# Kernel tuning notes

Hardware: AMD Instinct MI355X
Metric: run time of the kernel (lower is better)

Reference implementation:

```python
import jax, jax.numpy as jnp
from jax import lax
import numpy as np

D_X, D_Y, HID = 64, 1, 128
D_NODES = D_X + 2          # d_x + 2
D_IN = D_X + 1 + D_Y       # fc_in input dim
K_LANGEVIN, ETA = 20, 0.01
BATCH = 8192


def setup_inputs() -> dict:
    key = jax.random.key(0)
    ks = jax.random.split(key, 12)
    s = 0.05
    return {
        "x": jax.random.normal(ks[0], (BATCH, D_X), jnp.float32),
        "t": jnp.ones((BATCH, 1), jnp.float32),
        "B_param": s * jax.random.normal(ks[1], (D_NODES, D_NODES), jnp.float32),
        "W_in": s * jax.random.normal(ks[2], (D_IN, HID), jnp.float32),
        "b_in": jnp.zeros((HID,), jnp.float32),
        "WT1": s * jax.random.normal(ks[3], (HID, HID), jnp.float32),
        "bT1": jnp.zeros((HID,), jnp.float32),
        "WT2": s * jax.random.normal(ks[4], (HID, 1), jnp.float32),
        "bT2": jnp.zeros((1,), jnp.float32),
        "WY1": s * jax.random.normal(ks[5], (HID, HID), jnp.float32),
        "bY1": jnp.zeros((HID,), jnp.float32),
        "WY2": s * jax.random.normal(ks[6], (HID, 1), jnp.float32),
        "bY2": jnp.zeros((1,), jnp.float32),
    }


def _mask():
    m = jnp.ones((D_NODES, D_NODES), jnp.float32)
    m = m.at[-1, :D_X].set(0.0)          # last node has no incoming edges from x-nodes
    m = m * (1.0 - jnp.eye(D_NODES, dtype=jnp.float32))  # zero diagonal
    return m


def _energy(z, x, B_param, mask, W_in, b_in, WT1, bT1, WT2, bT2, WY1, bY1, WY2, bY2):
    # z = [t, y] : [B, 1 + d_y]
    A = jax.nn.sigmoid(B_param) * mask                       # [N, N]
    h0 = jnp.concatenate([x, z], axis=-1) @ W_in + b_in      # [B, H]
    h = jnp.broadcast_to(h0[:, None, :], (h0.shape[0], D_NODES, HID))  # repeat over nodes
    # MaskedGraphConv: h + (A @ h) / d_nodes, then ReLU (x2)
    h = jax.nn.relu(h + jnp.einsum('ij,bjd->bid', A, h) / D_NODES)
    h = jax.nn.relu(h + jnp.einsum('ij,bjd->bid', A, h) / D_NODES)
    eT = jax.nn.relu(h[:, -2] @ WT1 + bT1) @ WT2 + bT2       # [B, 1]
    eY = jax.nn.relu(h[:, -1] @ WY1 + bY1) @ WY2 + bY2       # [B, 1]
    return (eT + eY)[:, 0]                                   # [B]


def reference(x, t, B_param, W_in, b_in, WT1, bT1, WT2, bT2, WY1, bY1, WY2, bY2):
    mask = _mask()
    grad_E = jax.grad(lambda z: _energy(z, x, B_param, mask, W_in, b_in,
                                        WT1, bT1, WT2, bT2, WY1, bY1, WY2, bY2).sum())
    z0 = jnp.concatenate([t, jnp.zeros((x.shape[0], D_Y), x.dtype)], axis=-1)
    sqrt_eta = jnp.sqrt(jnp.float32(ETA))

    def step(z, k):
        g = grad_E(z)
        noise = jax.random.normal(k, z.shape, z.dtype)
        return z - 0.5 * ETA * g + sqrt_eta * noise, None

    keys = jax.random.split(jax.random.key(42), K_LANGEVIN)
    z_final, _ = lax.scan(step, z0, keys)
    return z_final[:, 1:]   # predicted y, [B, d_y]
```

## Files before the change

### kernel.cpp

```cpp
#include <hip/hip_runtime.h>
#include <stdint.h>

#define NBATCH 8192
#define HID    128
#define DXC    64
#define NN     66
#define NSTEP  20
#define MROWS  16
#define RSTR   136
#define DSTR   280

typedef __attribute__((ext_vector_type(8))) short short8;
typedef __attribute__((ext_vector_type(4))) float f32x4;

static __device__ __forceinline__ ushort f2bf(float f) {
  union { float f; uint32_t u; } v; v.f = f;
  uint32_t u = v.u;
  u += 0x7fffu + ((u >> 16) & 1u);
  return (ushort)(u >> 16);
}

__device__ __forceinline__ void tf2x32(uint32_t k1, uint32_t k2,
                                       uint32_t x0, uint32_t x1,
                                       uint32_t &o0, uint32_t &o1) {
  uint32_t k3 = k1 ^ k2 ^ 0x1BD11BDAu;
  x0 += k1; x1 += k2;
#define RND(r) do { x0 += x1; x1 = (x1 << (r)) | (x1 >> (32 - (r))); x1 ^= x0; } while (0)
  RND(13); RND(15); RND(26); RND(6);
  x0 += k2; x1 += k3 + 1u;
  RND(17); RND(29); RND(16); RND(24);
  x0 += k3; x1 += k1 + 2u;
  RND(13); RND(15); RND(26); RND(6);
  x0 += k1; x1 += k2 + 3u;
  RND(17); RND(29); RND(16); RND(24);
  x0 += k2; x1 += k3 + 4u;
  RND(13); RND(15); RND(26); RND(6);
  x0 += k3; x1 += k1 + 5u;
#undef RND
  o0 = x0; o1 = x1;
}

__device__ __forceinline__ float erfinv_f(float x) {
  float w = -log1pf(-x * x);
  float p1, p2;
  {
    float ww = w - 2.5f;
    float p = 2.81022636e-08f;
    p = fmaf(p, ww, 3.43273939e-07f);
    p = fmaf(p, ww, -3.5233877e-06f);
    p = fmaf(p, ww, -4.39150654e-06f);
    p = fmaf(p, ww, 0.00021858087f);
    p = fmaf(p, ww, -0.00125372503f);
    p = fmaf(p, ww, -0.00417768164f);
    p = fmaf(p, ww, 0.246640727f);
    p = fmaf(p, ww, 1.50140941f);
    p1 = p;
  }
  {
    float ww = sqrtf(w) - 3.0f;
    float p = -0.000200214257f;
    p = fmaf(p, ww, 0.000100950558f);
    p = fmaf(p, ww, 0.00134934322f);
    p = fmaf(p, ww, -0.00367342844f);
    p = fmaf(p, ww, 0.00573950773f);
    p = fmaf(p, ww, -0.0076224613f);
    p = fmaf(p, ww, 0.00943887047f);
    p = fmaf(p, ww, 1.00167406f);
    p = fmaf(p, ww, 2.83297682f);
    p2 = p;
  }
  float p = (w < 5.0f) ? p1 : p2;
  return p * x;
}

__device__ __forceinline__ float bits_to_normal(uint32_t bits) {
  float f = __uint_as_float((bits >> 9) | 0x3F800000u) - 1.0f;
  const float LO = -0.99999994f;
  float u = fmaxf(LO, fmaf(f, 2.0f, LO));
  return 1.41421356237f * erfinv_f(u);
}

__global__ __launch_bounds__(256) void prep_frags(const float* __restrict__ Bp,
                                                  const float* __restrict__ WT1,
                                                  const float* __restrict__ WY1,
                                                  ushort* __restrict__ frag) {
  __shared__ float cb[NN];
  __shared__ float dsc[2];
  int tid = threadIdx.x;
  if (tid < NN) {
    float rs = 0.f;
    for (int j = 0; j < NN; ++j) {
      if (j == tid) continue;
      if (tid == NN - 1 && j < DXC) continue;
      float v = Bp[tid * NN + j];
      rs += 1.f / (1.f + expf(-v));
    }
    cb[tid] = 1.f + rs / 66.f;
  }
  __syncthreads();
  if (tid < 2) {
    int i = 64 + tid;
    float s = 0.f;
    for (int j = 0; j < NN; ++j) {
      if (j == i) continue;
      if (i == NN - 1 && j < DXC) continue;
      float v = Bp[i * NN + j];
      s += (1.f / (1.f + expf(-v))) * cb[j];
    }
    dsc[tid] = cb[i] + s / 66.f;
  }
  __syncthreads();
  float d64 = dsc[0], d65 = dsc[1];

  int g = blockIdx.x * 256 + tid;
  int lane = g & 63, kt = (g >> 6) & 3, c = (g >> 8) & 7, mi = g >> 11;
  int r16 = lane & 15, q = lane >> 4;
  int bcol = c * 16 + r16;
  const float* W = (mi == 0 || mi == 2) ? WT1 : WY1;
  float d = (mi == 0 || mi == 2) ? d64 : d65;
  bool fwd = (mi < 2);
  ushort v[8];
#pragma unroll
  for (int j = 0; j < 8; ++j) {
    int a = kt * 32 + q * 8 + j;
    float val = fwd ? W[a * HID + bcol] : W[bcol * HID + a];
    v[j] = f2bf(d * val);
  }
  uint4 st;
  st.x = (uint32_t)v[0] | ((uint32_t)v[1] << 16);
  st.y = (uint32_t)v[2] | ((uint32_t)v[3] << 16);
  st.z = (uint32_t)v[4] | ((uint32_t)v[5] << 16);
  st.w = (uint32_t)v[6] | ((uint32_t)v[7] << 16);
  ((uint4*)frag)[g] = st;
}

__global__ __launch_bounds__(256, 2) void ebm_langevin(
    const float* __restrict__ x, const float* __restrict__ t_in,
    const float* __restrict__ W_in, const float* __restrict__ b_in,
    const float* __restrict__ bT1, const float* __restrict__ WT2,
    const float* __restrict__ bY1, const float* __restrict__ WY2,
    const ushort* __restrict__ fragw,
    float* __restrict__ out) {

  __shared__ __align__(16) ushort rT[MROWS * RSTR];
  __shared__ __align__(16) ushort duL[MROWS * DSTR];
  __shared__ float xs[MROWS * DXC];
  __shared__ float zt[MROWS], zy[MROWS];
  __shared__ float gpart[4][MROWS][2];
  __shared__ uint32_t skeys[NSTEP][2];

  const int tid  = threadIdx.x;
  const int lane = tid & 63;
  const int wv   = tid >> 6;
  const int r16  = lane & 15;
  const int q    = lane >> 4;
  const int brow0 = blockIdx.x * MROWS;

  const short8* fragp = reinterpret_cast<const short8*>(fragw);

  const int c0 = 2 * wv, c1 = 2 * wv + 1;
  const int n0 = c0 * 16 + r16, n1 = c1 * 16 + r16;
  const float bT1a = bT1[n0], bT1b = bT1[n1];
  const float bY1a = bY1[n0], bY1b = bY1[n1];
  const ushort wT2a = f2bf(WT2[n0]), wT2b = f2bf(WT2[n1]);
  const ushort wY2a = f2bf(WY2[n0]), wY2b = f2bf(WY2[n1]);
  const float wtA = W_in[64 * HID + n0], wtB = W_in[64 * HID + n1];
  const float wyA = W_in[65 * HID + n0], wyB = W_in[65 * HID + n1];

  const float2 wtk2 = ((const float2*)(W_in + 64 * HID))[lane];
  const float2 wyk2 = ((const float2*)(W_in + 65 * HID))[lane];

  ((float4*)xs)[tid] = ((const float4*)(x + (size_t)brow0 * DXC))[tid];
  if (tid < MROWS) { zt[tid] = t_in[brow0 + tid]; zy[tid] = 0.f; }
  if (tid < NSTEP) {
    uint32_t o0, o1;
    tf2x32(0u, 42u, 0u, (uint32_t)tid, o0, o1);
    skeys[tid][0] = o0; skeys[tid][1] = o1;
  }
  __syncthreads();

  float h0x_[4][2];
  {
    float2 b2 = ((const float2*)b_in)[lane];
#pragma unroll
    for (int m = 0; m < 4; ++m) { h0x_[m][0] = b2.x; h0x_[m][1] = b2.y; }
    for (int cc = 0; cc < DXC; ++cc) {
      float2 w2 = ((const float2*)(W_in + cc * HID))[lane];
#pragma unroll
      for (int m = 0; m < 4; ++m) {
        float xv = xs[(wv * 4 + m) * DXC + cc];
        h0x_[m][0] = fmaf(xv, w2.x, h0x_[m][0]);
        h0x_[m][1] = fmaf(xv, w2.y, h0x_[m][1]);
      }
    }
  }
  __syncthreads();

  for (int s = 0; s < NSTEP; ++s) {
#pragma unroll
    for (int m = 0; m < 4; ++m) {
      int mg = wv * 4 + m;
      float ztv = zt[mg], zyv = zy[mg];
      float h0 = fmaf(zyv, wyk2.x, fmaf(ztv, wtk2.x, h0x_[m][0]));
      float h1 = fmaf(zyv, wyk2.y, fmaf(ztv, wtk2.y, h0x_[m][1]));
      ushort lo = f2bf(fmaxf(h0, 0.f));
      ushort hi = f2bf(fmaxf(h1, 0.f));
      ((uint32_t*)rT)[mg * (RSTR / 2) + lane] = (uint32_t)lo | ((uint32_t)hi << 16);
    }
    __syncthreads();

    {
      short8 ar[4];
#pragma unroll
      for (int kt = 0; kt < 4; ++kt)
        ar[kt] = *reinterpret_cast<const short8*>(&rT[r16 * RSTR + kt * 32 + q * 8]);

      f32x4 aT0 = {0.f, 0.f, 0.f, 0.f}, aT1 = aT0, aY0 = aT0, aY1 = aT0;
#pragma unroll
      for (int kt = 0; kt < 4; ++kt) {
        aT0 = __builtin_amdgcn_mfma_f32_16x16x32_bf16(ar[kt], fragp[((0 * 8 + c0) * 4 + kt) * 64 + lane], aT0, 0, 0, 0);
        aT1 = __builtin_amdgcn_mfma_f32_16x16x32_bf16(ar[kt], fragp[((0 * 8 + c1) * 4 + kt) * 64 + lane], aT1, 0, 0, 0);
        aY0 = __builtin_amdgcn_mfma_f32_16x16x32_bf16(ar[kt], fragp[((1 * 8 + c0) * 4 + kt) * 64 + lane], aY0, 0, 0, 0);
        aY1 = __builtin_amdgcn_mfma_f32_16x16x32_bf16(ar[kt], fragp[((1 * 8 + c1) * 4 + kt) * 64 + lane], aY1, 0, 0, 0);
      }
#pragma unroll
      for (int reg = 0; reg < 4; ++reg) {
        int row = q * 4 + reg;
        duL[row * DSTR + n0]       = (aT0[reg] + bT1a > 0.f) ? wT2a : (ushort)0;
        duL[row * DSTR + n1]       = (aT1[reg] + bT1b > 0.f) ? wT2b : (ushort)0;
        duL[row * DSTR + 128 + n0] = (aY0[reg] + bY1a > 0.f) ? wY2a : (ushort)0;
        duL[row * DSTR + 128 + n1] = (aY1[reg] + bY1b > 0.f) ? wY2b : (ushort)0;
      }
    }
    __syncthreads();

    {
      short8 dt[4], dy[4];
#pragma unroll
      for (int kt = 0; kt < 4; ++kt) {
        dt[kt] = *reinterpret_cast<const short8*>(&duL[r16 * DSTR + kt * 32 + q * 8]);
        dy[kt] = *reinterpret_cast<const short8*>(&duL[r16 * DSTR + 128 + kt * 32 + q * 8]);
      }
      f32x4 g0 = {0.f, 0.f, 0.f, 0.f}, g1 = g0;
#pragma unroll
      for (int kt = 0; kt < 4; ++kt) {
        g0 = __builtin_amdgcn_mfma_f32_16x16x32_bf16(dt[kt], fragp[((2 * 8 + c0) * 4 + kt) * 64 + lane], g0, 0, 0, 0);
        g1 = __builtin_amdgcn_mfma_f32_16x16x32_bf16(dt[kt], fragp[((2 * 8 + c1) * 4 + kt) * 64 + lane], g1, 0, 0, 0);
      }
#pragma unroll
      for (int kt = 0; kt < 4; ++kt) {
        g0 = __builtin_amdgcn_mfma_f32_16x16x32_bf16(dy[kt], fragp[((3 * 8 + c0) * 4 + kt) * 64 + lane], g0, 0, 0, 0);
        g1 = __builtin_amdgcn_mfma_f32_16x16x32_bf16(dy[kt], fragp[((3 * 8 + c1) * 4 + kt) * 64 + lane], g1, 0, 0, 0);
      }
      float pt[4], py[4];
#pragma unroll
      for (int reg = 0; reg < 4; ++reg) {
        int row = q * 4 + reg;
        short rv0 = (short)rT[row * RSTR + n0];
        short rv1 = (short)rT[row * RSTR + n1];
        float v0 = (rv0 > 0) ? g0[reg] : 0.f;
        float v1 = (rv1 > 0) ? g1[reg] : 0.f;
        pt[reg] = fmaf(v0, wtA, v1 * wtB);
        py[reg] = fmaf(v0, wyA, v1 * wyB);
      }
#pragma unroll
      for (int reg = 0; reg < 4; ++reg) {
#pragma unroll
        for (int off = 1; off < 16; off <<= 1) {
          pt[reg] += __shfl_xor(pt[reg], off);
          py[reg] += __shfl_xor(py[reg], off);
        }
      }
      if (r16 == 0) {
#pragma unroll
        for (int reg = 0; reg < 4; ++reg) {
          gpart[wv][q * 4 + reg][0] = pt[reg];
          gpart[wv][q * 4 + reg][1] = py[reg];
        }
      }
    }
    __syncthreads();

    if (tid < MROWS) {
      float gt = gpart[0][tid][0] + gpart[1][tid][0] + gpart[2][tid][0] + gpart[3][tid][0];
      float gy = gpart[0][tid][1] + gpart[1][tid][1] + gpart[2][tid][1] + gpart[3][tid][1];
      uint32_t idx = (uint32_t)(2 * (brow0 + tid));
      uint32_t o0, o1;
      tf2x32(skeys[s][0], skeys[s][1], 0u, idx, o0, o1);
      float nt = bits_to_normal(o0 ^ o1);
      tf2x32(skeys[s][0], skeys[s][1], 0u, idx + 1u, o0, o1);
      float ny = bits_to_normal(o0 ^ o1);
      zt[tid] = (zt[tid] - 0.005f * gt) + 0.1f * nt;
      zy[tid] = (zy[tid] - 0.005f * gy) + 0.1f * ny;
    }
    __syncthreads();
  }

  if (tid < MROWS) out[brow0 + tid] = zy[tid];
}

extern "C" void kernel_launch(void* const* d_in, const int* in_sizes, int n_in,
                              void* d_out, int out_size, void* d_ws, size_t ws_size,
                              hipStream_t stream) {
  const float* x    = (const float*)d_in[0];
  const float* t_in = (const float*)d_in[1];
  const float* Bp   = (const float*)d_in[2];
  const float* W_in = (const float*)d_in[3];
  const float* b_in = (const float*)d_in[4];
  const float* WT1  = (const float*)d_in[5];
  const float* bT1  = (const float*)d_in[6];
  const float* WT2  = (const float*)d_in[7];
  const float* WY1  = (const float*)d_in[9];
  const float* bY1  = (const float*)d_in[10];
  const float* WY2  = (const float*)d_in[11];
  float* out = (float*)d_out;
  ushort* frag = (ushort*)d_ws;

  prep_frags<<<64, 256, 0, stream>>>(Bp, WT1, WY1, frag);
  ebm_langevin<<<NBATCH / MROWS, 256, 0, stream>>>(
      x, t_in, W_in, b_in, bT1, WT2, bY1, WY2, frag, out);
}
```

Measured before the change: 168.8 us.

## Fuse weight-fragment prep into Langevin kernel and hold B-fragments in registers

Removes the separate prep_frags launch. Every block now computes the graph-conv scale factors from B_param and builds its bf16 MFMA B-fragments for WT1/WY1 (forward and transposed) directly into registers, instead of reloading them from a global workspace on every Langevin step. This drops one kernel launch and the per-step global fragment loads. In exchange it adds redundant per-block sigmoid and weight-conversion work, 32 short8 registers per thread that may hurt occupancy or spill, and uncoalesced strided reads of WT1/WY1.

```diff
diff --git a/kernel.cpp b/kernel.cpp
--- a/kernel.cpp
+++ b/kernel.cpp
@@ -80,13 +80,39 @@
   return 1.41421356237f * erfinv_f(u);
 }
 
-__global__ __launch_bounds__(256) void prep_frags(const float* __restrict__ Bp,
-                                                  const float* __restrict__ WT1,
-                                                  const float* __restrict__ WY1,
-                                                  ushort* __restrict__ frag) {
+__global__ __launch_bounds__(256, 2) void ebm_fused(
+    const float* __restrict__ x, const float* __restrict__ t_in,
+    const float* __restrict__ Bp,
+    const float* __restrict__ W_in, const float* __restrict__ b_in,
+    const float* __restrict__ WT1, const float* __restrict__ bT1,
+    const float* __restrict__ WT2,
+    const float* __restrict__ WY1, const float* __restrict__ bY1,
+    const float* __restrict__ WY2,
+    float* __restrict__ out) {
+
+  __shared__ __align__(16) ushort rT[MROWS * RSTR];
+  __shared__ __align__(16) ushort duL[MROWS * DSTR];
+  __shared__ float xs[MROWS * DXC];
+  __shared__ float zt[MROWS], zy[MROWS];
+  __shared__ float gpart[4][MROWS][2];
+  __shared__ uint32_t skeys[NSTEP][2];
   __shared__ float cb[NN];
   __shared__ float dsc[2];
-  int tid = threadIdx.x;
+
+  const int tid  = threadIdx.x;
+  const int lane = tid & 63;
+  const int wv   = tid >> 6;
+  const int r16  = lane & 15;
+  const int q    = lane >> 4;
+  const int brow0 = blockIdx.x * MROWS;
+
+  ((float4*)xs)[tid] = ((const float4*)(x + (size_t)brow0 * DXC))[tid];
+  if (tid < MROWS) { zt[tid] = t_in[brow0 + tid]; zy[tid] = 0.f; }
+  if (tid < NSTEP) {
+    uint32_t o0, o1;
+    tf2x32(0u, 42u, 0u, (uint32_t)tid, o0, o1);
+    skeys[tid][0] = o0; skeys[tid][1] = o1;
+  }
   if (tid < NN) {
     float rs = 0.f;
     for (int j = 0; j < NN; ++j) {
@@ -110,74 +136,46 @@
     dsc[tid] = cb[i] + s / 66.f;
   }
   __syncthreads();
-  float d64 = dsc[0], d65 = dsc[1];
-
-  int g = blockIdx.x * 256 + tid;
-  int lane = g & 63, kt = (g >> 6) & 3, c = (g >> 8) & 7, mi = g >> 11;
-  int r16 = lane & 15, q = lane >> 4;
-  int bcol = c * 16 + r16;
-  const float* W = (mi == 0 || mi == 2) ? WT1 : WY1;
-  float d = (mi == 0 || mi == 2) ? d64 : d65;
-  bool fwd = (mi < 2);
-  ushort v[8];
-#pragma unroll
-  for (int j = 0; j < 8; ++j) {
-    int a = kt * 32 + q * 8 + j;
-    float val = fwd ? W[a * HID + bcol] : W[bcol * HID + a];
-    v[j] = f2bf(d * val);
-  }
-  uint4 st;
-  st.x = (uint32_t)v[0] | ((uint32_t)v[1] << 16);
-  st.y = (uint32_t)v[2] | ((uint32_t)v[3] << 16);
-  st.z = (uint32_t)v[4] | ((uint32_t)v[5] << 16);
-  st.w = (uint32_t)v[6] | ((uint32_t)v[7] << 16);
-  ((uint4*)frag)[g] = st;
-}
-
-__global__ __launch_bounds__(256, 2) void ebm_langevin(
-    const float* __restrict__ x, const float* __restrict__ t_in,
-    const float* __restrict__ W_in, const float* __restrict__ b_in,
-    const float* __restrict__ bT1, const float* __restrict__ WT2,
-    const float* __restrict__ bY1, const float* __restrict__ WY2,
-    const ushort* __restrict__ fragw,
-    float* __restrict__ out) {
-
-  __shared__ __align__(16) ushort rT[MROWS * RSTR];
-  __shared__ __align__(16) ushort duL[MROWS * DSTR];
-  __shared__ float xs[MROWS * DXC];
-  __shared__ float zt[MROWS], zy[MROWS];
-  __shared__ float gpart[4][MROWS][2];
-  __shared__ uint32_t skeys[NSTEP][2];
-
-  const int tid  = threadIdx.x;
-  const int lane = tid & 63;
-  const int wv   = tid >> 6;
-  const int r16  = lane & 15;
-  const int q    = lane >> 4;
-  const int brow0 = blockIdx.x * MROWS;
-
-  const short8* fragp = reinterpret_cast<const short8*>(fragw);
-
-  const int c0 = 2 * wv, c1 = 2 * wv + 1;
-  const int n0 = c0 * 16 + r16, n1 = c1 * 16 + r16;
+  const float d64 = dsc[0], d65 = dsc[1];
+
+  const int n0 = 32 * wv + r16, n1 = n0 + 16;
   const float bT1a = bT1[n0], bT1b = bT1[n1];
   const float bY1a = bY1[n0], bY1b = bY1[n1];
   const ushort wT2a = f2bf(WT2[n0]), wT2b = f2bf(WT2[n1]);
   const ushort wY2a = f2bf(WY2[n0]), wY2b = f2bf(WY2[n1]);
   const float wtA = W_in[64 * HID + n0], wtB = W_in[64 * HID + n1];
   const float wyA = W_in[65 * HID + n0], wyB = W_in[65 * HID + n1];
-
   const float2 wtk2 = ((const float2*)(W_in + 64 * HID))[lane];
   const float2 wyk2 = ((const float2*)(W_in + 65 * HID))[lane];
 
-  ((float4*)xs)[tid] = ((const float4*)(x + (size_t)brow0 * DXC))[tid];
-  if (tid < MROWS) { zt[tid] = t_in[brow0 + tid]; zy[tid] = 0.f; }
-  if (tid < NSTEP) {
-    uint32_t o0, o1;
-    tf2x32(0u, 42u, 0u, (uint32_t)tid, o0, o1);
-    skeys[tid][0] = o0; skeys[tid][1] = o1;
-  }
-  __syncthreads();
+  short8 fT0[4], fT1[4], fY0[4], fY1[4];
+  short8 hT0[4], hT1[4], hY0[4], hY1[4];
+#pragma unroll
+  for (int kt = 0; kt < 4; ++kt) {
+    const int kb = kt * 32 + q * 8;
+    short8 a0, a1, b0, b1;
+#pragma unroll
+    for (int j = 0; j < 8; ++j) {
+      a0[j] = (short)f2bf(d64 * WT1[(kb + j) * HID + n0]);
+      a1[j] = (short)f2bf(d64 * WT1[(kb + j) * HID + n1]);
+      b0[j] = (short)f2bf(d65 * WY1[(kb + j) * HID + n0]);
+      b1[j] = (short)f2bf(d65 * WY1[(kb + j) * HID + n1]);
+    }
+    fT0[kt] = a0; fT1[kt] = a1; fY0[kt] = b0; fY1[kt] = b1;
+    const float* pT0 = WT1 + (size_t)n0 * HID + kb;
+    const float* pT1 = WT1 + (size_t)n1 * HID + kb;
+    const float* pY0 = WY1 + (size_t)n0 * HID + kb;
+    const float* pY1 = WY1 + (size_t)n1 * HID + kb;
+    short8 c0v, c1v, e0, e1;
+#pragma unroll
+    for (int j = 0; j < 8; ++j) {
+      c0v[j] = (short)f2bf(d64 * pT0[j]);
+      c1v[j] = (short)f2bf(d64 * pT1[j]);
+      e0[j]  = (short)f2bf(d65 * pY0[j]);
+      e1[j]  = (short)f2bf(d65 * pY1[j]);
+    }
+    hT0[kt] = c0v; hT1[kt] = c1v; hY0[kt] = e0; hY1[kt] = e1;
+  }
 
   float h0x_[4][2];
   {
@@ -218,10 +216,10 @@
       f32x4 aT0 = {0.f, 0.f, 0.f, 0.f}, aT1 = aT0, aY0 = aT0, aY1 = aT0;
 #pragma unroll
       for (int kt = 0; kt < 4; ++kt) {
-        aT0 = __builtin_amdgcn_mfma_f32_16x16x32_bf16(ar[kt], fragp[((0 * 8 + c0) * 4 + kt) * 64 + lane], aT0, 0, 0, 0);
-        aT1 = __builtin_amdgcn_mfma_f32_16x16x32_bf16(ar[kt], fragp[((0 * 8 + c1) * 4 + kt) * 64 + lane], aT1, 0, 0, 0);
-        aY0 = __builtin_amdgcn_mfma_f32_16x16x32_bf16(ar[kt], fragp[((1 * 8 + c0) * 4 + kt) * 64 + lane], aY0, 0, 0, 0);
-        aY1 = __builtin_amdgcn_mfma_f32_16x16x32_bf16(ar[kt], fragp[((1 * 8 + c1) * 4 + kt) * 64 + lane], aY1, 0, 0, 0);
+        aT0 = __builtin_amdgcn_mfma_f32_16x16x32_bf16(ar[kt], fT0[kt], aT0, 0, 0, 0);
+        aT1 = __builtin_amdgcn_mfma_f32_16x16x32_bf16(ar[kt], fT1[kt], aT1, 0, 0, 0);
+        aY0 = __builtin_amdgcn_mfma_f32_16x16x32_bf16(ar[kt], fY0[kt], aY0, 0, 0, 0);
+        aY1 = __builtin_amdgcn_mfma_f32_16x16x32_bf16(ar[kt], fY1[kt], aY1, 0, 0, 0);
       }
 #pragma unroll
       for (int reg = 0; reg < 4; ++reg) {
@@ -235,22 +233,23 @@
     __syncthreads();
 
     {
-      short8 dt[4], dy[4];
+      short8 d8[4];
+#pragma unroll
+      for (int kt = 0; kt < 4; ++kt)
+        d8[kt] = *reinterpret_cast<const short8*>(&duL[r16 * DSTR + kt * 32 + q * 8]);
+      f32x4 g0 = {0.f, 0.f, 0.f, 0.f}, g1 = g0;
 #pragma unroll
       for (int kt = 0; kt < 4; ++kt) {
-        dt[kt] = *reinterpret_cast<const short8*>(&duL[r16 * DSTR + kt * 32 + q * 8]);
-        dy[kt] = *reinterpret_cast<const short8*>(&duL[r16 * DSTR + 128 + kt * 32 + q * 8]);
-      }
-      f32x4 g0 = {0.f, 0.f, 0.f, 0.f}, g1 = g0;
+        g0 = __builtin_amdgcn_mfma_f32_16x16x32_bf16(d8[kt], hT0[kt], g0, 0, 0, 0);
+        g1 = __builtin_amdgcn_mfma_f32_16x16x32_bf16(d8[kt], hT1[kt], g1, 0, 0, 0);
+      }
+#pragma unroll
+      for (int kt = 0; kt < 4; ++kt)
+        d8[kt] = *reinterpret_cast<const short8*>(&duL[r16 * DSTR + 128 + kt * 32 + q * 8]);
 #pragma unroll
       for (int kt = 0; kt < 4; ++kt) {
-        g0 = __builtin_amdgcn_mfma_f32_16x16x32_bf16(dt[kt], fragp[((2 * 8 + c0) * 4 + kt) * 64 + lane], g0, 0, 0, 0);
-        g1 = __builtin_amdgcn_mfma_f32_16x16x32_bf16(dt[kt], fragp[((2 * 8 + c1) * 4 + kt) * 64 + lane], g1, 0, 0, 0);
-      }
-#pragma unroll
-      for (int kt = 0; kt < 4; ++kt) {
-        g0 = __builtin_amdgcn_mfma_f32_16x16x32_bf16(dy[kt], fragp[((3 * 8 + c0) * 4 + kt) * 64 + lane], g0, 0, 0, 0);
-        g1 = __builtin_amdgcn_mfma_f32_16x16x32_bf16(dy[kt], fragp[((3 * 8 + c1) * 4 + kt) * 64 + lane], g1, 0, 0, 0);
+        g0 = __builtin_amdgcn_mfma_f32_16x16x32_bf16(d8[kt], hY0[kt], g0, 0, 0, 0);
+        g1 = __builtin_amdgcn_mfma_f32_16x16x32_bf16(d8[kt], hY1[kt], g1, 0, 0, 0);
       }
       float pt[4], py[4];
 #pragma unroll
@@ -314,9 +313,7 @@
   const float* bY1  = (const float*)d_in[10];
   const float* WY2  = (const float*)d_in[11];
   float* out = (float*)d_out;
-  ushort* frag = (ushort*)d_ws;
-
-  prep_frags<<<64, 256, 0, stream>>>(Bp, WT1, WY1, frag);
-  ebm_langevin<<<NBATCH / MROWS, 256, 0, stream>>>(
-      x, t_in, W_in, b_in, bT1, WT2, bY1, WY2, frag, out);
-}
+
+  ebm_fused<<<NBATCH / MROWS, 256, 0, stream>>>(
+      x, t_in, Bp, W_in, b_in, WT1, bT1, WT2, WY1, bY1, WY2, out);
+}
```

Result: slower. 189.0 us (+12.0%).

## Process each 16-row tile with a single wavefront instead of four

Applied to the files above, without the earlier changes.

Reworks the Langevin kernel so one 64-thread wavefront handles a 16-row tile and computes all 8 column blocks itself, replacing the four-wave split. The cross-wave gradient reduction through shared memory and most block barriers go away. Noise for all steps is precomputed into shared memory up front, and z is kept in registers. In exchange each wave issues four times as many MFMAs serially and holds more registers (h0x grows to 32 floats), which can lower per-wave latency hiding. Occupancy now depends on LDS and register use.

```diff
diff --git a/kernel.cpp b/kernel.cpp
--- a/kernel.cpp
+++ b/kernel.cpp
@@ -134,7 +134,7 @@
   ((uint4*)frag)[g] = st;
 }
 
-__global__ __launch_bounds__(256, 2) void ebm_langevin(
+__global__ __launch_bounds__(64) void ebm_wave(
     const float* __restrict__ x, const float* __restrict__ t_in,
     const float* __restrict__ W_in, const float* __restrict__ b_in,
     const float* __restrict__ bT1, const float* __restrict__ WT2,
@@ -144,68 +144,85 @@
 
   __shared__ __align__(16) ushort rT[MROWS * RSTR];
   __shared__ __align__(16) ushort duL[MROWS * DSTR];
-  __shared__ float xs[MROWS * DXC];
-  __shared__ float zt[MROWS], zy[MROWS];
-  __shared__ float gpart[4][MROWS][2];
+  __shared__ __align__(16) float xs[MROWS * DXC];
+  __shared__ float nbuf[NSTEP * 2 * MROWS];
   __shared__ uint32_t skeys[NSTEP][2];
 
   const int tid  = threadIdx.x;
-  const int lane = tid & 63;
-  const int wv   = tid >> 6;
-  const int r16  = lane & 15;
-  const int q    = lane >> 4;
+  const int r16  = tid & 15;
+  const int q    = tid >> 4;
   const int brow0 = blockIdx.x * MROWS;
 
   const short8* fragp = reinterpret_cast<const short8*>(fragw);
 
-  const int c0 = 2 * wv, c1 = 2 * wv + 1;
-  const int n0 = c0 * 16 + r16, n1 = c1 * 16 + r16;
-  const float bT1a = bT1[n0], bT1b = bT1[n1];
-  const float bY1a = bY1[n0], bY1b = bY1[n1];
-  const ushort wT2a = f2bf(WT2[n0]), wT2b = f2bf(WT2[n1]);
-  const ushort wY2a = f2bf(WY2[n0]), wY2b = f2bf(WY2[n1]);
-  const float wtA = W_in[64 * HID + n0], wtB = W_in[64 * HID + n1];
-  const float wyA = W_in[65 * HID + n0], wyB = W_in[65 * HID + n1];
-
-  const float2 wtk2 = ((const float2*)(W_in + 64 * HID))[lane];
-  const float2 wyk2 = ((const float2*)(W_in + 65 * HID))[lane];
-
-  ((float4*)xs)[tid] = ((const float4*)(x + (size_t)brow0 * DXC))[tid];
-  if (tid < MROWS) { zt[tid] = t_in[brow0 + tid]; zy[tid] = 0.f; }
   if (tid < NSTEP) {
     uint32_t o0, o1;
     tf2x32(0u, 42u, 0u, (uint32_t)tid, o0, o1);
     skeys[tid][0] = o0; skeys[tid][1] = o1;
   }
+  for (int i = tid; i < MROWS * DXC / 4; i += 64)
+    ((float4*)xs)[i] = ((const float4*)(x + (size_t)brow0 * DXC))[i];
   __syncthreads();
 
-  float h0x_[4][2];
-  {
-    float2 b2 = ((const float2*)b_in)[lane];
-#pragma unroll
-    for (int m = 0; m < 4; ++m) { h0x_[m][0] = b2.x; h0x_[m][1] = b2.y; }
-    for (int cc = 0; cc < DXC; ++cc) {
-      float2 w2 = ((const float2*)(W_in + cc * HID))[lane];
-#pragma unroll
-      for (int m = 0; m < 4; ++m) {
-        float xv = xs[(wv * 4 + m) * DXC + cc];
-        h0x_[m][0] = fmaf(xv, w2.x, h0x_[m][0]);
-        h0x_[m][1] = fmaf(xv, w2.y, h0x_[m][1]);
-      }
-    }
+  for (int f = tid; f < NSTEP * 2 * MROWS; f += 64) {
+    int s = f >> 5, rr = f & 31;
+    uint32_t idx = (uint32_t)(2 * (brow0 + (rr >> 1)) + (rr & 1));
+    uint32_t o0, o1;
+    tf2x32(skeys[s][0], skeys[s][1], 0u, idx, o0, o1);
+    nbuf[f] = bits_to_normal(o0 ^ o1);
+  }
+
+  float wtC[8], wyC[8], bT1C[8], bY1C[8];
+  ushort wT2C[8], wY2C[8];
+#pragma unroll
+  for (int c = 0; c < 8; ++c) {
+    int col = 16 * c + r16;
+    wtC[c]  = W_in[64 * HID + col];
+    wyC[c]  = W_in[65 * HID + col];
+    bT1C[c] = bT1[col];
+    bY1C[c] = bY1[col];
+    wT2C[c] = f2bf(WT2[col]);
+    wY2C[c] = f2bf(WY2[col]);
+  }
+
+  float h0x[4][8];
+#pragma unroll
+  for (int c = 0; c < 8; ++c) {
+    float bv = b_in[16 * c + r16];
+#pragma unroll
+    for (int reg = 0; reg < 4; ++reg) h0x[reg][c] = bv;
+  }
+  for (int cc = 0; cc < DXC; ++cc) {
+    float w[8];
+#pragma unroll
+    for (int c = 0; c < 8; ++c) w[c] = W_in[cc * HID + 16 * c + r16];
+#pragma unroll
+    for (int reg = 0; reg < 4; ++reg) {
+      float xv = xs[(q * 4 + reg) * DXC + cc];
+#pragma unroll
+      for (int c = 0; c < 8; ++c) h0x[reg][c] = fmaf(xv, w[c], h0x[reg][c]);
+    }
+  }
+
+  float zt[4], zy[4];
+#pragma unroll
+  for (int reg = 0; reg < 4; ++reg) {
+    zt[reg] = t_in[brow0 + q * 4 + reg];
+    zy[reg] = 0.f;
   }
   __syncthreads();
 
   for (int s = 0; s < NSTEP; ++s) {
-#pragma unroll
-    for (int m = 0; m < 4; ++m) {
-      int mg = wv * 4 + m;
-      float ztv = zt[mg], zyv = zy[mg];
-      float h0 = fmaf(zyv, wyk2.x, fmaf(ztv, wtk2.x, h0x_[m][0]));
-      float h1 = fmaf(zyv, wyk2.y, fmaf(ztv, wtk2.y, h0x_[m][1]));
-      ushort lo = f2bf(fmaxf(h0, 0.f));
-      ushort hi = f2bf(fmaxf(h1, 0.f));
-      ((uint32_t*)rT)[mg * (RSTR / 2) + lane] = (uint32_t)lo | ((uint32_t)hi << 16);
+    uint32_t mb = 0;
+#pragma unroll
+    for (int reg = 0; reg < 4; ++reg) {
+#pragma unroll
+      for (int c = 0; c < 8; ++c) {
+        float h = fmaf(zy[reg], wyC[c], fmaf(zt[reg], wtC[c], h0x[reg][c]));
+        ushort rb = f2bf(fmaxf(h, 0.f));
+        rT[(q * 4 + reg) * RSTR + 16 * c + r16] = rb;
+        mb |= ((short)rb > 0 ? 1u : 0u) << (reg * 8 + c);
+      }
     }
     __syncthreads();
 
@@ -215,88 +232,74 @@
       for (int kt = 0; kt < 4; ++kt)
         ar[kt] = *reinterpret_cast<const short8*>(&rT[r16 * RSTR + kt * 32 + q * 8]);
 
-      f32x4 aT0 = {0.f, 0.f, 0.f, 0.f}, aT1 = aT0, aY0 = aT0, aY1 = aT0;
+#pragma unroll
+      for (int c = 0; c < 8; ++c) {
+        f32x4 aT = {0.f, 0.f, 0.f, 0.f}, aY = aT;
+#pragma unroll
+        for (int kt = 0; kt < 4; ++kt) {
+          aT = __builtin_amdgcn_mfma_f32_16x16x32_bf16(ar[kt], fragp[((0 * 8 + c) * 4 + kt) * 64 + tid], aT, 0, 0, 0);
+          aY = __builtin_amdgcn_mfma_f32_16x16x32_bf16(ar[kt], fragp[((1 * 8 + c) * 4 + kt) * 64 + tid], aY, 0, 0, 0);
+        }
+#pragma unroll
+        for (int reg = 0; reg < 4; ++reg) {
+          int rr = q * 4 + reg;
+          duL[rr * DSTR + 16 * c + r16]       = (aT[reg] + bT1C[c] > 0.f) ? wT2C[c] : (ushort)0;
+          duL[rr * DSTR + 128 + 16 * c + r16] = (aY[reg] + bY1C[c] > 0.f) ? wY2C[c] : (ushort)0;
+        }
+      }
+    }
+    __syncthreads();
+
+    float pt[4] = {0.f, 0.f, 0.f, 0.f}, py[4] = {0.f, 0.f, 0.f, 0.f};
+    {
+      short8 dT[4], dY[4];
 #pragma unroll
       for (int kt = 0; kt < 4; ++kt) {
-        aT0 = __builtin_amdgcn_mfma_f32_16x16x32_bf16(ar[kt], fragp[((0 * 8 + c0) * 4 + kt) * 64 + lane], aT0, 0, 0, 0);
-        aT1 = __builtin_amdgcn_mfma_f32_16x16x32_bf16(ar[kt], fragp[((0 * 8 + c1) * 4 + kt) * 64 + lane], aT1, 0, 0, 0);
-        aY0 = __builtin_amdgcn_mfma_f32_16x16x32_bf16(ar[kt], fragp[((1 * 8 + c0) * 4 + kt) * 64 + lane], aY0, 0, 0, 0);
-        aY1 = __builtin_amdgcn_mfma_f32_16x16x32_bf16(ar[kt], fragp[((1 * 8 + c1) * 4 + kt) * 64 + lane], aY1, 0, 0, 0);
-      }
-#pragma unroll
-      for (int reg = 0; reg < 4; ++reg) {
-        int row = q * 4 + reg;
-        duL[row * DSTR + n0]       = (aT0[reg] + bT1a > 0.f) ? wT2a : (ushort)0;
-        duL[row * DSTR + n1]       = (aT1[reg] + bT1b > 0.f) ? wT2b : (ushort)0;
-        duL[row * DSTR + 128 + n0] = (aY0[reg] + bY1a > 0.f) ? wY2a : (ushort)0;
-        duL[row * DSTR + 128 + n1] = (aY1[reg] + bY1b > 0.f) ? wY2b : (ushort)0;
-      }
+        dT[kt] = *reinterpret_cast<const short8*>(&duL[r16 * DSTR + kt * 32 + q * 8]);
+        dY[kt] = *reinterpret_cast<const short8*>(&duL[r16 * DSTR + 128 + kt * 32 + q * 8]);
+      }
+#pragma unroll
+      for (int c = 0; c < 8; ++c) {
+        f32x4 g = {0.f, 0.f, 0.f, 0.f};
+#pragma unroll
+        for (int kt = 0; kt < 4; ++kt)
+          g = __builtin_amdgcn_mfma_f32_16x16x32_bf16(dT[kt], fragp[((2 * 8 + c) * 4 + kt) * 64 + tid], g, 0, 0, 0);
+#pragma unroll
+        for (int kt = 0; kt < 4; ++kt)
+          g = __builtin_amdgcn_mfma_f32_16x16x32_bf16(dY[kt], fragp[((3 * 8 + c) * 4 + kt) * 64 + tid], g, 0, 0, 0);
+#pragma unroll
+        for (int reg = 0; reg < 4; ++reg) {
+          float v = ((mb >> (reg * 8 + c)) & 1u) ? g[reg] : 0.f;
+          pt[reg] = fmaf(v, wtC[c], pt[reg]);
+          py[reg] = fmaf(v, wyC[c], py[reg]);
+        }
+      }
+    }
+#pragma unroll
+    for (int reg = 0; reg < 4; ++reg) {
+#pragma unroll
+      for (int off = 1; off < 16; off <<= 1) {
+        pt[reg] += __shfl_xor(pt[reg], off);
+        py[reg] += __shfl_xor(py[reg], off);
+      }
+    }
+
+#pragma unroll
+    for (int reg = 0; reg < 4; ++reg) {
+      int row = q * 4 + reg;
+      float nt = nbuf[s * 32 + 2 * row];
+      float ny = nbuf[s * 32 + 2 * row + 1];
+      zt[reg] = (zt[reg] - 0.005f * pt[reg]) + 0.1f * nt;
+      zy[reg] = (zy[reg] - 0.005f * py[reg]) + 0.1f * ny;
     }
     __syncthreads();
-
-    {
-      short8 dt[4], dy[4];
-#pragma unroll
-      for (int kt = 0; kt < 4; ++kt) {
-        dt[kt] = *reinterpret_cast<const short8*>(&duL[r16 * DSTR + kt * 32 + q * 8]);
-        dy[kt] = *reinterpret_cast<const short8*>(&duL[r16 * DSTR + 128 + kt * 32 + q * 8]);
-      }
-      f32x4 g0 = {0.f, 0.f, 0.f, 0.f}, g1 = g0;
-#pragma unroll
-      for (int kt = 0; kt < 4; ++kt) {
-        g0 = __builtin_amdgcn_mfma_f32_16x16x32_bf16(dt[kt], fragp[((2 * 8 + c0) * 4 + kt) * 64 + lane], g0, 0, 0, 0);
-        g1 = __builtin_amdgcn_mfma_f32_16x16x32_bf16(dt[kt], fragp[((2 * 8 + c1) * 4 + kt) * 64 + lane], g1, 0, 0, 0);
-      }
-#pragma unroll
-      for (int kt = 0; kt < 4; ++kt) {
-        g0 = __builtin_amdgcn_mfma_f32_16x16x32_bf16(dy[kt], fragp[((3 * 8 + c0) * 4 + kt) * 64 + lane], g0, 0, 0, 0);
-        g1 = __builtin_amdgcn_mfma_f32_16x16x32_bf16(dy[kt], fragp[((3 * 8 + c1) * 4 + kt) * 64 + lane], g1, 0, 0, 0);
-      }
-      float pt[4], py[4];
-#pragma unroll
-      for (int reg = 0; reg < 4; ++reg) {
-        int row = q * 4 + reg;
-        short rv0 = (short)rT[row * RSTR + n0];
-        short rv1 = (short)rT[row * RSTR + n1];
-        float v0 = (rv0 > 0) ? g0[reg] : 0.f;
-        float v1 = (rv1 > 0) ? g1[reg] : 0.f;
-        pt[reg] = fmaf(v0, wtA, v1 * wtB);
-        py[reg] = fmaf(v0, wyA, v1 * wyB);
-      }
-#pragma unroll
-      for (int reg = 0; reg < 4; ++reg) {
-#pragma unroll
-        for (int off = 1; off < 16; off <<= 1) {
-          pt[reg] += __shfl_xor(pt[reg], off);
-          py[reg] += __shfl_xor(py[reg], off);
-        }
-      }
-      if (r16 == 0) {
-#pragma unroll
-        for (int reg = 0; reg < 4; ++reg) {
-          gpart[wv][q * 4 + reg][0] = pt[reg];
-          gpart[wv][q * 4 + reg][1] = py[reg];
-        }
-      }
-    }
-    __syncthreads();
-
-    if (tid < MROWS) {
-      float gt = gpart[0][tid][0] + gpart[1][tid][0] + gpart[2][tid][0] + gpart[3][tid][0];
-      float gy = gpart[0][tid][1] + gpart[1][tid][1] + gpart[2][tid][1] + gpart[3][tid][1];
-      uint32_t idx = (uint32_t)(2 * (brow0 + tid));
-      uint32_t o0, o1;
-      tf2x32(skeys[s][0], skeys[s][1], 0u, idx, o0, o1);
-      float nt = bits_to_normal(o0 ^ o1);
-      tf2x32(skeys[s][0], skeys[s][1], 0u, idx + 1u, o0, o1);
-      float ny = bits_to_normal(o0 ^ o1);
-      zt[tid] = (zt[tid] - 0.005f * gt) + 0.1f * nt;
-      zy[tid] = (zy[tid] - 0.005f * gy) + 0.1f * ny;
-    }
-    __syncthreads();
-  }
-
-  if (tid < MROWS) out[brow0 + tid] = zy[tid];
+  }
+
+  if (r16 == 0) {
+#pragma unroll
+    for (int reg = 0; reg < 4; ++reg)
+      out[brow0 + q * 4 + reg] = zy[reg];
+  }
 }
 
 extern "C" void kernel_launch(void* const* d_in, const int* in_sizes, int n_in,
@@ -317,6 +320,6 @@
   ushort* frag = (ushort*)d_ws;
 
   prep_frags<<<64, 256, 0, stream>>>(Bp, WT1, WY1, frag);
-  ebm_langevin<<<NBATCH / MROWS, 256, 0, stream>>>(
+  ebm_wave<<<NBATCH / MROWS, 64, 0, stream>>>(
       x, t_in, W_in, b_in, bT1, WT2, bY1, WY2, frag, out);
 }
```

Measured after the change: 308.4 us. +82.7%, slower.
